# Kernel tuning notes

Measured on AMD Instinct MI355X. Metric: run time of the kernel, lower is better.

## Reference

```python
import jax, jax.numpy as jnp
import numpy as np
jax.config.update("jax_enable_x64", True)

B, S, E, H, L = 2, 1024, 768, 8, 8
FF, V = 2048, 32000
NT, REAL = 1, 512  # n_thoughts_taken, real_token_count


def _ln(x, g, b, eps=1e-5):
    m = jnp.mean(x, axis=-1, keepdims=True)
    v = jnp.var(x, axis=-1, keepdims=True)
    return (x - m) / jnp.sqrt(v + eps) * g + b


def setup_inputs() -> dict:
    key = jax.random.key(0)
    ks = jax.random.split(key, 12)
    f32 = jnp.float32
    rn = lambda k, shp, s=0.02: jax.random.normal(k, shp, f32) * s
    return {
        "x": jax.random.normal(ks[0], (B, S, E), f32),
        "tpe": rn(ks[1], (NT + 1, E)),
        "Wqkv": rn(ks[2], (L, 3 * E, E)),
        "bqkv": jnp.zeros((L, 3 * E), f32),
        "W1": rn(ks[3], (L, FF, E)),
        "b1": jnp.zeros((L, FF), f32),
        "W2": rn(ks[4], (L, E, FF)),
        "b2": jnp.zeros((L, E), f32),
        "g1": jnp.ones((L, E), f32),
        "be1": jnp.zeros((L, E), f32),
        "g2": jnp.ones((L, E), f32),
        "be2": jnp.zeros((L, E), f32),
        "gf": jnp.ones((E,), f32),
        "bf": jnp.zeros((E,), f32),
        "Wp1": rn(ks[5], (FF, E)),
        "bp1": jnp.zeros((FF,), f32),
        "Wp2": rn(ks[6], (V, FF)),
        "bp2": jnp.zeros((V,), f32),
        "Wv1": rn(ks[7], (FF, E)),
        "bv1": jnp.zeros((FF,), f32),
        "Wv2": rn(ks[8], (1, FF)),
        "bv2": jnp.zeros((1,), f32),
        "n_thoughts_taken": NT,
        "real_token_count": REAL,
    }


def reference(x, tpe, Wqkv, bqkv, W1, b1, W2, b2, g1, be1, g2, be2, gf, bf,
              Wp1, bp1, Wp2, bp2, Wv1, bv1, Wv2, bv2,
              n_thoughts_taken, real_token_count):
    Bs, Sq, Em = x.shape
    bs = int(n_thoughts_taken) + 1          # per-thought block size
    real = int(real_token_count)
    dh = Em // H

    # ---- DualPositionalEncoding (dropout=0) ----
    pos = np.arange(real)[:, None]
    div = np.exp(np.arange(0, Em, 2) * (-np.log(10000.0) / Em))
    pe = np.zeros((real, Em), np.float32)
    pe[:, 0::2] = np.sin(pos * div)
    pe[:, 1::2] = np.cos(pos * div)
    xb = x[:, :real * bs].reshape(Bs, real, bs, Em)
    xb = xb + jnp.asarray(pe)[None, :, None, :] + tpe[None, None, :bs, :]
    h = xb.reshape(Bs, real * bs, Em)
    pad = Sq - real * bs
    if pad > 0:
        h = jnp.pad(h, ((0, 0), (0, pad), (0, 0)))

    # ---- block-causal mask. NOTE: the original adds the BOOL mask to the
    # fp64 scores, so masked positions get +1.0 (not -inf). Faithful. ----
    i = np.arange(Sq)
    tok = i // bs
    p = i % bs
    M = ((tok[:, None] == tok[None, :]) & (p[None, :] >= p[:, None])) | \
        ((p[:, None] == 0) & (i[None, :] > i[:, None]) & (i[None, :] < real * bs))
    bias = jnp.asarray((M.T == 0).astype(np.float64))  # [S, S]
    scale = 1.0 / np.sqrt(dh)

    def layer(hc, params):
        Wq, bq, w1, b1_, w2, b2_, g1_, be1_, g2_, be2_ = params
        h64 = hc.astype(jnp.float64)
        qkv = h64 @ Wq.astype(jnp.float64).T + bq.astype(jnp.float64)
        q, k, v = jnp.split(qkv, 3, axis=-1)
        heads = lambda t: t.reshape(Bs, Sq, H, dh).transpose(0, 2, 1, 3)
        q, k, v = heads(q), heads(k), heads(v)
        scores = jnp.einsum('bhqd,bhkd->bhqk', q, k) * scale + bias
        w = jax.nn.softmax(scores, axis=-1)
        o = jnp.einsum('bhqk,bhkd->bhqd', w, v)
        o = o.transpose(0, 2, 1, 3).reshape(Bs, Sq, Em).astype(hc.dtype)
        # NOTE: original skips the attention out_proj entirely. Faithful.
        hc = _ln(hc + o, g1_, be1_)
        ff = jax.nn.gelu(hc @ w1.T + b1_, approximate=False) @ w2.T + b2_
        hc = _ln(hc + ff, g2_, be2_)
        return jnp.nan_to_num(hc), None

    h, _ = jax.lax.scan(layer, h, (Wqkv, bqkv, W1, b1, W2, b2, g1, be1, g2, be2))
    h = _ln(h, gf, bf)  # TransformerEncoder final norm

    act_idx = jnp.arange(real) * bs + n_thoughts_taken
    a = h[:, act_idx]  # [B, real, E]
    policy = jax.nn.gelu(a @ Wp1.T + bp1, approximate=False) @ Wp2.T + bp2
    value = jax.nn.gelu(a @ Wv1.T + bv1, approximate=False) @ Wv2.T + bv2
    return policy, value
```

## Files before the change

### kernel.cpp

```cpp
#include <hip/hip_runtime.h>
#include <math.h>

#define BB    2
#define SS    1024
#define EE    768
#define NH    8
#define DHD   96
#define NL    8
#define FFD   2048
#define VD    32000
#define REALC 512
#define MTOK  (BB*SS)
#define MACTN (BB*REALC)
#define QKVW  (3*EE)

#define QB 64
#define KB 64
#define KS_LD 104
#define VT_LD 72
#define P_LD  72

typedef __attribute__((ext_vector_type(8))) short bf16x8;
typedef __attribute__((ext_vector_type(4))) float f32x4;

static __device__ __forceinline__ float gelu_exact(float x) {
    return 0.5f * x * (1.0f + erff(x * 0.7071067811865476f));
}
static __device__ __forceinline__ unsigned short f2bf(float f) {
    unsigned int u = __builtin_bit_cast(unsigned int, f);
    unsigned int r = u + 0x7FFFu + ((u >> 16) & 1u);
    return (unsigned short)(r >> 16);
}
static __device__ __forceinline__ float bf2f(unsigned short u) {
    union { unsigned int i; float f; } v; v.i = ((unsigned int)u) << 16; return v.f;
}

#define GLDS16(gp, lp) __builtin_amdgcn_global_load_lds( \
    (const __attribute__((address_space(1))) void*)(gp), \
    (__attribute__((address_space(3))) void*)(lp), 16, 0, 0)

__global__ __launch_bounds__(256) void f2b_kernel(const float* __restrict__ src,
                                                  unsigned short* __restrict__ dst, int n4) {
    int i = blockIdx.x * 256 + threadIdx.x;
    if (i >= n4) return;
    float4 v = ((const float4*)src)[i];
    ushort4 o;
    o.x = f2bf(v.x); o.y = f2bf(v.y); o.z = f2bf(v.z); o.w = f2bf(v.w);
    ((ushort4*)dst)[i] = o;
}

__global__ __launch_bounds__(256) void embed_kernel(const float* __restrict__ x,
                                                    const float* __restrict__ tpe,
                                                    float* __restrict__ h,
                                                    unsigned short* __restrict__ hb) {
    int idx = blockIdx.x * 256 + threadIdx.x;
    if (idx >= MTOK * EE) return;
    int e = idx % EE;
    int tok = idx / EE;
    int s = tok & (SS - 1);
    int r = s >> 1;
    int p = s & 1;
    int k2 = (e >> 1) * 2;
    double div = exp((double)k2 * (-9.210340371976184 / (double)EE));
    double ang = (double)r * div;
    float pe = (e & 1) ? (float)cos(ang) : (float)sin(ang);
    float v = x[idx] + pe + tpe[p * EE + e];
    h[idx] = v;
    hb[idx] = f2bf(v);
}

template<int MODE>
__global__ __launch_bounds__(256) void gemm_bf16_kernel(
    const unsigned short* __restrict__ A, const unsigned short* __restrict__ W,
    const float* __restrict__ bias, float* __restrict__ Cf,
    unsigned short* __restrict__ Cb, unsigned short* __restrict__ CvT,
    int M, int N, int K, int ldc) {
    __shared__ unsigned short As[128 * 64];
    __shared__ unsigned short Ws[128 * 64];
    const int bm = blockIdx.y * 128;
    const int bn = blockIdx.x * 128;
    const int t = threadIdx.x;
    const int wave = t >> 6;
    const int lane = t & 63;
    const int wm = (wave >> 1) * 64;
    const int wn = (wave & 1) * 64;
    f32x4 acc[4][4] = {};

    const int srow = wave * 32 + (lane >> 3);
    const int scol = (lane & 7) * 8;
    const unsigned short* gA = A + (size_t)(bm + srow) * K + scol;
    const unsigned short* gW = W + (size_t)(bn + srow) * K + scol;

    for (int k0 = 0; k0 < K; k0 += 64) {
        __syncthreads();
#pragma unroll
        for (int i = 0; i < 4; ++i) {
            GLDS16(gA + (size_t)(i * 8) * K + k0, &As[(wave * 32 + i * 8) * 64]);
            GLDS16(gW + (size_t)(i * 8) * K + k0, &Ws[(wave * 32 + i * 8) * 64]);
        }
        __syncthreads();
#pragma unroll
        for (int ks = 0; ks < 2; ++ks) {
            bf16x8 a[4], b[4];
#pragma unroll
            for (int mi = 0; mi < 4; ++mi)
                a[mi] = *(const bf16x8*)&As[(wm + mi * 16 + (lane & 15)) * 64 + ks * 32 + (lane >> 4) * 8];
#pragma unroll
            for (int ni = 0; ni < 4; ++ni)
                b[ni] = *(const bf16x8*)&Ws[(wn + ni * 16 + (lane & 15)) * 64 + ks * 32 + (lane >> 4) * 8];
#pragma unroll
            for (int mi = 0; mi < 4; ++mi)
#pragma unroll
                for (int ni = 0; ni < 4; ++ni)
                    acc[mi][ni] = __builtin_amdgcn_mfma_f32_16x16x32_bf16(
                        a[mi], b[ni], acc[mi][ni], 0, 0, 0);
        }
    }

    const bool vpart = (MODE == 1) && (bn >= 2 * EE);
#pragma unroll
    for (int mi = 0; mi < 4; ++mi) {
#pragma unroll
        for (int ni = 0; ni < 4; ++ni) {
            const int c = bn + wn + ni * 16 + (lane & 15);
            const float bv = bias[c];
            const int rwb = bm + wm + mi * 16 + (lane >> 4) * 4;
            if (vpart) {
                ushort4 pk;
                pk.x = f2bf(acc[mi][ni][0] + bv);
                pk.y = f2bf(acc[mi][ni][1] + bv);
                pk.z = f2bf(acc[mi][ni][2] + bv);
                pk.w = f2bf(acc[mi][ni][3] + bv);
                *(ushort4*)&CvT[(size_t)(c - 2 * EE) * MTOK + rwb] = pk;
            } else {
#pragma unroll
                for (int r = 0; r < 4; ++r) {
                    float v = acc[mi][ni][r] + bv;
                    if (MODE == 3) {
                        v = gelu_exact(v);
                        Cb[(size_t)(rwb + r) * ldc + c] = f2bf(v);
                    } else if (MODE == 1) {
                        Cb[(size_t)(rwb + r) * ldc + c] = f2bf(v);
                    } else {
                        Cf[(size_t)(rwb + r) * ldc + c] = v;
                    }
                }
            }
        }
    }
}

__global__ __launch_bounds__(256, 2) void gemm_policy_kernel(
    const unsigned short* __restrict__ A, const unsigned short* __restrict__ W,
    const float* __restrict__ bias, float* __restrict__ C) {
    const int id = blockIdx.x;
    const int xcd = id & 7;
    const int rest = id >> 3;
    const int mt = rest & 7;
    const int nt = (rest >> 3) * 8 + xcd;
    if (nt >= VD / 256) return;
    const int bm = mt * 128;
    const int bn = nt * 256;
    const int K = FFD;

    __shared__ unsigned short As[128 * 64];
    __shared__ unsigned short Bs[256 * 64];
    const int t = threadIdx.x;
    const int w = t >> 6;
    const int lane = t & 63;
    const int wm = (w >> 1) * 64;
    const int wn = (w & 1) * 128;
    f32x4 acc[4][8] = {};

    const int rr8 = (w << 3) + (lane >> 3);
    const int cc8 = (lane & 7) * 8;
    const unsigned short* gA = A + (size_t)(bm + rr8) * K + cc8;
    const unsigned short* gB = W + (size_t)(bn + rr8) * K + cc8;

    for (int k0 = 0; k0 < K; k0 += 64) {
        __syncthreads();
#pragma unroll
        for (int i = 0; i < 4; ++i)
            GLDS16(gA + (size_t)(i * 32) * K + k0, &As[((w << 3) + i * 32) * 64]);
#pragma unroll
        for (int i = 0; i < 8; ++i)
            GLDS16(gB + (size_t)(i * 32) * K + k0, &Bs[((w << 3) + i * 32) * 64]);
        __syncthreads();
#pragma unroll
        for (int ks = 0; ks < 2; ++ks) {
            bf16x8 a[4], b[8];
#pragma unroll
            for (int mi = 0; mi < 4; ++mi)
                a[mi] = *(const bf16x8*)&As[(wm + mi * 16 + (lane & 15)) * 64 + ks * 32 + (lane >> 4) * 8];
#pragma unroll
            for (int ni = 0; ni < 8; ++ni)
                b[ni] = *(const bf16x8*)&Bs[(wn + ni * 16 + (lane & 15)) * 64 + ks * 32 + (lane >> 4) * 8];
#pragma unroll
            for (int mi = 0; mi < 4; ++mi)
#pragma unroll
                for (int ni = 0; ni < 8; ++ni)
                    acc[mi][ni] = __builtin_amdgcn_mfma_f32_16x16x32_bf16(
                        a[mi], b[ni], acc[mi][ni], 0, 0, 0);
        }
    }
#pragma unroll
    for (int mi = 0; mi < 4; ++mi) {
#pragma unroll
        for (int ni = 0; ni < 8; ++ni) {
            const int c = bn + wn + ni * 16 + (lane & 15);
            const float bv = bias[c];
            const int rwb = bm + wm + mi * 16 + (lane >> 4) * 4;
#pragma unroll
            for (int r = 0; r < 4; ++r)
                C[(size_t)(rwb + r) * VD + c] = acc[mi][ni][r] + bv;
        }
    }
}

__global__ __launch_bounds__(256) void attn_mfma_kernel(
    const unsigned short* __restrict__ qkvb,
    const unsigned short* __restrict__ vT,
    float* __restrict__ o) {
    __shared__ unsigned short Ks[KB * KS_LD];
    __shared__ unsigned short VTs[DHD * VT_LD];
    __shared__ unsigned short Ps[QB * P_LD];

    const int bq = blockIdx.x * QB;
    const int hh = blockIdx.y & 7;
    const int b  = blockIdx.y >> 3;
    const int t = threadIdx.x;
    const int w = t >> 6;
    const int lane = t & 63;
    const int lr = lane >> 4;
    const int lc = lane & 15;
    const float scale = 0.10206207261596577f;

    bf16x8 qa[3];
    {
        const unsigned short* qrow = qkvb + (size_t)(b * SS + bq + w * 16 + lc) * QKVW + hh * DHD;
#pragma unroll
        for (int ks = 0; ks < 3; ++ks)
            qa[ks] = *(const bf16x8*)(qrow + ks * 32 + lr * 8);
    }

    f32x4 acc_o[6] = {};
    float m_st[4], l_st[4];
#pragma unroll
    for (int r = 0; r < 4; ++r) { m_st[r] = -1e30f; l_st[r] = 0.f; }
    const int q_row = lr << 2;

    for (int kt = 0; kt < SS / KB; ++kt) {
        __syncthreads();
#pragma unroll
        for (int it = 0; it < 3; ++it) {
            int flat = it * 256 + t;
            int kr = flat / 12;
            int d8 = (flat % 12) * 8;
            *(bf16x8*)&Ks[kr * KS_LD + d8] =
                *(const bf16x8*)&qkvb[(size_t)(b * SS + kt * KB + kr) * QKVW + EE + hh * DHD + d8];
            int d  = flat >> 3;
            int k8 = (flat & 7) * 8;
            *(bf16x8*)&VTs[d * VT_LD + k8] =
                *(const bf16x8*)&vT[(size_t)(hh * DHD + d) * MTOK + b * SS + kt * KB + k8];
        }
        __syncthreads();

        f32x4 sfr[4] = {};
#pragma unroll
        for (int nf = 0; nf < 4; ++nf) {
#pragma unroll
            for (int ks = 0; ks < 3; ++ks) {
                bf16x8 kb = *(const bf16x8*)&Ks[(nf * 16 + lc) * KS_LD + ks * 32 + lr * 8];
                sfr[nf] = __builtin_amdgcn_mfma_f32_16x16x32_bf16(qa[ks], kb, sfr[nf], 0, 0, 0);
            }
        }
        const int kbase = kt * KB;
#pragma unroll
        for (int nf = 0; nf < 4; ++nf) {
            const int k = kbase + nf * 16 + lc;
#pragma unroll
            for (int r = 0; r < 4; ++r) {
                const int q = bq + w * 16 + q_row + r;
                bool allowed = (((k >> 1) == (q >> 1)) && ((q & 1) >= (k & 1))) ||
                               (((k & 1) == 0) && (q > k));
                sfr[nf][r] = sfr[nf][r] * scale + (allowed ? 0.f : 1.f);
            }
        }
        float corr[4];
#pragma unroll
        for (int r = 0; r < 4; ++r) {
            float v = fmaxf(fmaxf(sfr[0][r], sfr[1][r]), fmaxf(sfr[2][r], sfr[3][r]));
            v = fmaxf(v, __shfl_xor(v, 1)); v = fmaxf(v, __shfl_xor(v, 2));
            v = fmaxf(v, __shfl_xor(v, 4)); v = fmaxf(v, __shfl_xor(v, 8));
            float mn = fmaxf(m_st[r], v);
            corr[r] = __expf(m_st[r] - mn);
            m_st[r] = mn;
        }
        float rsum[4] = {0.f, 0.f, 0.f, 0.f};
#pragma unroll
        for (int nf = 0; nf < 4; ++nf) {
#pragma unroll
            for (int r = 0; r < 4; ++r) {
                float p = __expf(sfr[nf][r] - m_st[r]);
                rsum[r] += p;
                Ps[(w * 16 + q_row + r) * P_LD + nf * 16 + lc] = f2bf(p);
            }
        }
#pragma unroll
        for (int r = 0; r < 4; ++r) {
            float v = rsum[r];
            v += __shfl_xor(v, 1); v += __shfl_xor(v, 2);
            v += __shfl_xor(v, 4); v += __shfl_xor(v, 8);
            l_st[r] = l_st[r] * corr[r] + v;
        }
#pragma unroll
        for (int nf = 0; nf < 6; ++nf)
#pragma unroll
            for (int r = 0; r < 4; ++r)
                acc_o[nf][r] *= corr[r];
#pragma unroll
        for (int ks2 = 0; ks2 < 2; ++ks2) {
            bf16x8 pa = *(const bf16x8*)&Ps[(w * 16 + lc) * P_LD + ks2 * 32 + lr * 8];
#pragma unroll
            for (int nf = 0; nf < 6; ++nf) {
                bf16x8 vb = *(const bf16x8*)&VTs[(nf * 16 + lc) * VT_LD + ks2 * 32 + lr * 8];
                acc_o[nf] = __builtin_amdgcn_mfma_f32_16x16x32_bf16(pa, vb, acc_o[nf], 0, 0, 0);
            }
        }
    }
#pragma unroll
    for (int nf = 0; nf < 6; ++nf) {
#pragma unroll
        for (int r = 0; r < 4; ++r) {
            const int q = bq + w * 16 + q_row + r;
            o[(size_t)(b * SS + q) * EE + hh * DHD + nf * 16 + lc] = acc_o[nf][r] / l_st[r];
        }
    }
}

template<bool GATHER>
__global__ __launch_bounds__(256) void ln_kernel(const float* __restrict__ a,
                                                 const float* __restrict__ res,
                                                 const float* __restrict__ g,
                                                 const float* __restrict__ beta,
                                                 float* __restrict__ outf,
                                                 unsigned short* __restrict__ outb) {
    __shared__ float rs[256], rs2[256];
    const int row = blockIdx.x;
    const int t = threadIdx.x;
    int src = row;
    if (GATHER) src = (row >> 9) * SS + ((row & 511) << 1) + 1;
    const float* pa = a + (size_t)src * EE;
    const float* pr = res ? res + (size_t)src * EE : nullptr;
    float x[3];
    float s = 0.f, s2 = 0.f;
#pragma unroll
    for (int i = 0; i < 3; ++i) {
        int e = t + i * 256;
        float v = pa[e] + (pr ? pr[e] : 0.f);
        x[i] = v; s += v; s2 += v * v;
    }
    rs[t] = s; rs2[t] = s2; __syncthreads();
    for (int k = 128; k > 0; k >>= 1) {
        if (t < k) { rs[t] += rs[t + k]; rs2[t] += rs2[t + k]; }
        __syncthreads();
    }
    const float mean = rs[0] * (1.0f / EE);
    const float var  = rs2[0] * (1.0f / EE) - mean * mean;
    const float rstd = 1.0f / sqrtf(var + 1e-5f);
#pragma unroll
    for (int i = 0; i < 3; ++i) {
        int e = t + i * 256;
        float v = (x[i] - mean) * rstd * g[e] + beta[e];
        if (isnan(v)) v = 0.f;
        if (outf) outf[(size_t)row * EE + e] = v;
        if (outb) outb[(size_t)row * EE + e] = f2bf(v);
    }
}

__global__ __launch_bounds__(256) void value2_kernel(const unsigned short* __restrict__ v1,
                                                     const float* __restrict__ Wv2,
                                                     const float* __restrict__ bv2,
                                                     float* __restrict__ out) {
    __shared__ float red[256];
    const int row = blockIdx.x;
    const int t = threadIdx.x;
    const unsigned short* pr = v1 + (size_t)row * FFD;
    float s = 0.f;
    for (int i = t; i < FFD; i += 256) s = fmaf(bf2f(pr[i]), Wv2[i], s);
    red[t] = s; __syncthreads();
    for (int k = 128; k > 0; k >>= 1) {
        if (t < k) red[t] += red[t + k];
        __syncthreads();
    }
    if (t == 0) out[row] = red[0] + bv2[0];
}

extern "C" void kernel_launch(void* const* d_in, const int* in_sizes, int n_in,
                              void* d_out, int out_size, void* d_ws, size_t ws_size,
                              hipStream_t stream) {
    const float* x    = (const float*)d_in[0];
    const float* tpe  = (const float*)d_in[1];
    const float* Wqkv = (const float*)d_in[2];
    const float* bqkv = (const float*)d_in[3];
    const float* W1   = (const float*)d_in[4];
    const float* b1   = (const float*)d_in[5];
    const float* W2   = (const float*)d_in[6];
    const float* b2   = (const float*)d_in[7];
    const float* g1   = (const float*)d_in[8];
    const float* be1  = (const float*)d_in[9];
    const float* g2   = (const float*)d_in[10];
    const float* be2  = (const float*)d_in[11];
    const float* gf   = (const float*)d_in[12];
    const float* bf   = (const float*)d_in[13];
    const float* Wp1  = (const float*)d_in[14];
    const float* bp1  = (const float*)d_in[15];
    const float* Wp2  = (const float*)d_in[16];
    const float* bp2  = (const float*)d_in[17];
    const float* Wv1  = (const float*)d_in[18];
    const float* bv1  = (const float*)d_in[19];
    const float* Wv2  = (const float*)d_in[20];
    const float* bv2  = (const float*)d_in[21];

    float* ws  = (float*)d_ws;
    float* h   = ws;
    float* o   = h  + (size_t)MTOK * EE;
    float* hc  = o  + (size_t)MTOK * EE;
    float* ff2 = hc + (size_t)MTOK * EE;
    unsigned short* bws = (unsigned short*)(ff2 + (size_t)MTOK * EE);
    unsigned short* h_bf    = bws;
    unsigned short* hc_bf   = h_bf    + (size_t)MTOK * EE;
    unsigned short* ff1_bf  = hc_bf   + (size_t)MTOK * EE;
    unsigned short* act_bf  = ff1_bf  + (size_t)MTOK * FFD;
    unsigned short* p1_bf   = act_bf  + (size_t)MACTN * EE;
    unsigned short* qkv_bf  = p1_bf   + (size_t)MACTN * FFD;
    unsigned short* vT      = qkv_bf  + (size_t)MTOK * QKVW;
    unsigned short* wq_all  = vT      + (size_t)EE * MTOK;
    unsigned short* w1_all  = wq_all  + (size_t)NL * QKVW * EE;
    unsigned short* w2_all  = w1_all  + (size_t)NL * FFD * EE;
    unsigned short* wp1_bf  = w2_all  + (size_t)NL * EE * FFD;
    unsigned short* wv1_bf  = wp1_bf  + (size_t)FFD * EE;
    unsigned short* wp2_bf  = wv1_bf  + (size_t)FFD * EE;

    float* pol = (float*)d_out;
    float* val = (float*)d_out + (size_t)MACTN * VD;

    const int C256 = 256;
#define NBLK(n) (((n) + 255) / 256)
#define CONV(src, dst, n) f2b_kernel<<<NBLK((n) / 4), C256, 0, stream>>>(src, dst, (int)((n) / 4))

    embed_kernel<<<NBLK(MTOK * EE), C256, 0, stream>>>(x, tpe, h, h_bf);

    CONV(Wqkv, wq_all, (size_t)NL * QKVW * EE);
    CONV(W1,   w1_all, (size_t)NL * FFD * EE);
    CONV(W2,   w2_all, (size_t)NL * EE * FFD);
    CONV(Wp1,  wp1_bf, (size_t)FFD * EE);
    CONV(Wv1,  wv1_bf, (size_t)FFD * EE);
    CONV(Wp2,  wp2_bf, (size_t)VD * FFD);

    for (int l = 0; l < NL; ++l) {
        gemm_bf16_kernel<1><<<dim3(QKVW / 128, MTOK / 128), C256, 0, stream>>>(
            h_bf, wq_all + (size_t)l * QKVW * EE, bqkv + (size_t)l * QKVW,
            nullptr, qkv_bf, vT, MTOK, QKVW, EE, QKVW);
        attn_mfma_kernel<<<dim3(SS / QB, BB * NH), C256, 0, stream>>>(qkv_bf, vT, o);
        ln_kernel<false><<<MTOK, C256, 0, stream>>>(h, o, g1 + l * EE, be1 + l * EE, hc, hc_bf);
        gemm_bf16_kernel<3><<<dim3(FFD / 128, MTOK / 128), C256, 0, stream>>>(
            hc_bf, w1_all + (size_t)l * FFD * EE, b1 + (size_t)l * FFD,
            nullptr, ff1_bf, nullptr, MTOK, FFD, EE, FFD);
        gemm_bf16_kernel<0><<<dim3(EE / 128, MTOK / 128), C256, 0, stream>>>(
            ff1_bf, w2_all + (size_t)l * EE * FFD, b2 + (size_t)l * EE,
            ff2, nullptr, nullptr, MTOK, EE, FFD, EE);
        ln_kernel<false><<<MTOK, C256, 0, stream>>>(hc, ff2, g2 + l * EE, be2 + l * EE, h, h_bf);
    }

    ln_kernel<true><<<MACTN, C256, 0, stream>>>(h, nullptr, gf, bf, nullptr, act_bf);

    gemm_bf16_kernel<3><<<dim3(FFD / 128, MACTN / 128), C256, 0, stream>>>(
        act_bf, wp1_bf, bp1, nullptr, p1_bf, nullptr, MACTN, FFD, EE, FFD);
    gemm_policy_kernel<<<1024, C256, 0, stream>>>(p1_bf, wp2_bf, bp2, pol);

    gemm_bf16_kernel<3><<<dim3(FFD / 128, MACTN / 128), C256, 0, stream>>>(
        act_bf, wv1_bf, bv1, nullptr, p1_bf, nullptr, MACTN, FFD, EE, FFD);
    value2_kernel<<<MACTN, C256, 0, stream>>>(p1_bf, Wv2, bv2, val);
#undef CONV
#undef NBLK
}
```

Measured before the change: 1.589 ms.

## Merge weight conversions into one kernel and fuse policy/value head GEMMs

Six separate fp32-to-bf16 weight conversion launches are replaced by a single kernel that picks its source by index range. The policy and value first-layer GEMMs become one GEMM of width 2*FFD. This relies on Wp1 and Wv1 sitting next to each other in the bf16 buffer, with the two biases copied into a concatenated bias array. The policy GEMM occupancy hint is raised from 2 to 3, which may force register spilling. The goal is fewer launches and better GPU fill on the small head GEMMs, at the cost of strided A reads in the downstream kernels.

```diff
diff --git a/kernel.cpp b/kernel.cpp
--- a/kernel.cpp
+++ b/kernel.cpp
@@ -39,11 +39,34 @@
     (const __attribute__((address_space(1))) void*)(gp), \
     (__attribute__((address_space(3))) void*)(lp), 16, 0, 0)
 
-__global__ __launch_bounds__(256) void f2b_kernel(const float* __restrict__ src,
-                                                  unsigned short* __restrict__ dst, int n4) {
+#define CN0 (NL*QKVW*EE)
+#define CN1 (NL*FFD*EE)
+#define CN2 (NL*EE*FFD)
+#define CN3 (FFD*EE)
+#define CN4 (FFD*EE)
+#define CN5 (VD*FFD)
+#define CB0 (CN0/4)
+#define CB1 (CB0 + CN1/4)
+#define CB2 (CB1 + CN2/4)
+#define CB3 (CB2 + CN3/4)
+#define CB4 (CB3 + CN4/4)
+#define CB5 (CB4 + CN5/4)
+
+__global__ __launch_bounds__(256) void convall_kernel(
+    const float* __restrict__ s0, const float* __restrict__ s1,
+    const float* __restrict__ s2, const float* __restrict__ s3,
+    const float* __restrict__ s4, const float* __restrict__ s5,
+    unsigned short* __restrict__ dst) {
     int i = blockIdx.x * 256 + threadIdx.x;
-    if (i >= n4) return;
-    float4 v = ((const float4*)src)[i];
+    const float* src;
+    int loc;
+    if      (i < CB0) { src = s0; loc = i; }
+    else if (i < CB1) { src = s1; loc = i - CB0; }
+    else if (i < CB2) { src = s2; loc = i - CB1; }
+    else if (i < CB3) { src = s3; loc = i - CB2; }
+    else if (i < CB4) { src = s4; loc = i - CB3; }
+    else              { src = s5; loc = i - CB4; }
+    float4 v = ((const float4*)src)[loc];
     ushort4 o;
     o.x = f2bf(v.x); o.y = f2bf(v.y); o.z = f2bf(v.z); o.w = f2bf(v.w);
     ((ushort4*)dst)[i] = o;
@@ -150,9 +173,9 @@
     }
 }
 
-__global__ __launch_bounds__(256, 2) void gemm_policy_kernel(
+__global__ __launch_bounds__(256, 3) void gemm_policy_kernel(
     const unsigned short* __restrict__ A, const unsigned short* __restrict__ W,
-    const float* __restrict__ bias, float* __restrict__ C) {
+    const float* __restrict__ bias, float* __restrict__ C, int lda) {
     const int id = blockIdx.x;
     const int xcd = id & 7;
     const int rest = id >> 3;
@@ -174,14 +197,14 @@
 
     const int rr8 = (w << 3) + (lane >> 3);
     const int cc8 = (lane & 7) * 8;
-    const unsigned short* gA = A + (size_t)(bm + rr8) * K + cc8;
+    const unsigned short* gA = A + (size_t)(bm + rr8) * lda + cc8;
     const unsigned short* gB = W + (size_t)(bn + rr8) * K + cc8;
 
     for (int k0 = 0; k0 < K; k0 += 64) {
         __syncthreads();
 #pragma unroll
         for (int i = 0; i < 4; ++i)
-            GLDS16(gA + (size_t)(i * 32) * K + k0, &As[((w << 3) + i * 32) * 64]);
+            GLDS16(gA + (size_t)(i * 32) * lda + k0, &As[((w << 3) + i * 32) * 64]);
 #pragma unroll
         for (int i = 0; i < 8; ++i)
             GLDS16(gB + (size_t)(i * 32) * K + k0, &Bs[((w << 3) + i * 32) * 64]);
@@ -381,11 +404,11 @@
 __global__ __launch_bounds__(256) void value2_kernel(const unsigned short* __restrict__ v1,
                                                      const float* __restrict__ Wv2,
                                                      const float* __restrict__ bv2,
-                                                     float* __restrict__ out) {
+                                                     float* __restrict__ out, int ld) {
     __shared__ float red[256];
     const int row = blockIdx.x;
     const int t = threadIdx.x;
-    const unsigned short* pr = v1 + (size_t)row * FFD;
+    const unsigned short* pr = v1 + (size_t)row * ld;
     float s = 0.f;
     for (int i = t; i < FFD; i += 256) s = fmaf(bf2f(pr[i]), Wv2[i], s);
     red[t] = s; __syncthreads();
@@ -427,36 +450,35 @@
     float* o   = h  + (size_t)MTOK * EE;
     float* hc  = o  + (size_t)MTOK * EE;
     float* ff2 = hc + (size_t)MTOK * EE;
-    unsigned short* bws = (unsigned short*)(ff2 + (size_t)MTOK * EE);
+    float* bias_cat = ff2 + (size_t)MTOK * EE;
+    unsigned short* bws = (unsigned short*)(bias_cat + 4096);
     unsigned short* h_bf    = bws;
     unsigned short* hc_bf   = h_bf    + (size_t)MTOK * EE;
     unsigned short* ff1_bf  = hc_bf   + (size_t)MTOK * EE;
     unsigned short* act_bf  = ff1_bf  + (size_t)MTOK * FFD;
-    unsigned short* p1_bf   = act_bf  + (size_t)MACTN * EE;
-    unsigned short* qkv_bf  = p1_bf   + (size_t)MACTN * FFD;
+    unsigned short* p1v1_bf = act_bf  + (size_t)MACTN * EE;
+    unsigned short* qkv_bf  = p1v1_bf + (size_t)MACTN * 2 * FFD;
     unsigned short* vT      = qkv_bf  + (size_t)MTOK * QKVW;
     unsigned short* wq_all  = vT      + (size_t)EE * MTOK;
-    unsigned short* w1_all  = wq_all  + (size_t)NL * QKVW * EE;
-    unsigned short* w2_all  = w1_all  + (size_t)NL * FFD * EE;
-    unsigned short* wp1_bf  = w2_all  + (size_t)NL * EE * FFD;
-    unsigned short* wv1_bf  = wp1_bf  + (size_t)FFD * EE;
-    unsigned short* wp2_bf  = wv1_bf  + (size_t)FFD * EE;
+    unsigned short* w1_all  = wq_all  + (size_t)CN0;
+    unsigned short* w2_all  = w1_all  + (size_t)CN1;
+    unsigned short* wp1_bf  = w2_all  + (size_t)CN2;
+    unsigned short* wv1_bf  = wp1_bf  + (size_t)CN3;
+    unsigned short* wp2_bf  = wv1_bf  + (size_t)CN4;
+    (void)wv1_bf;
 
     float* pol = (float*)d_out;
     float* val = (float*)d_out + (size_t)MACTN * VD;
 
     const int C256 = 256;
 #define NBLK(n) (((n) + 255) / 256)
-#define CONV(src, dst, n) f2b_kernel<<<NBLK((n) / 4), C256, 0, stream>>>(src, dst, (int)((n) / 4))
 
     embed_kernel<<<NBLK(MTOK * EE), C256, 0, stream>>>(x, tpe, h, h_bf);
 
-    CONV(Wqkv, wq_all, (size_t)NL * QKVW * EE);
-    CONV(W1,   w1_all, (size_t)NL * FFD * EE);
-    CONV(W2,   w2_all, (size_t)NL * EE * FFD);
-    CONV(Wp1,  wp1_bf, (size_t)FFD * EE);
-    CONV(Wv1,  wv1_bf, (size_t)FFD * EE);
-    CONV(Wp2,  wp2_bf, (size_t)VD * FFD);
+    convall_kernel<<<CB5 / 256, C256, 0, stream>>>(Wqkv, W1, W2, Wp1, Wv1, Wp2, wq_all);
+
+    hipMemcpyAsync(bias_cat,        bp1, FFD * sizeof(float), hipMemcpyDeviceToDevice, stream);
+    hipMemcpyAsync(bias_cat + FFD,  bv1, FFD * sizeof(float), hipMemcpyDeviceToDevice, stream);
 
     for (int l = 0; l < NL; ++l) {
         gemm_bf16_kernel<1><<<dim3(QKVW / 128, MTOK / 128), C256, 0, stream>>>(
@@ -475,13 +497,11 @@
 
     ln_kernel<true><<<MACTN, C256, 0, stream>>>(h, nullptr, gf, bf, nullptr, act_bf);
 
-    gemm_bf16_kernel<3><<<dim3(FFD / 128, MACTN / 128), C256, 0, stream>>>(
-        act_bf, wp1_bf, bp1, nullptr, p1_bf, nullptr, MACTN, FFD, EE, FFD);
-    gemm_policy_kernel<<<1024, C256, 0, stream>>>(p1_bf, wp2_bf, bp2, pol);
-
-    gemm_bf16_kernel<3><<<dim3(FFD / 128, MACTN / 128), C256, 0, stream>>>(
-        act_bf, wv1_bf, bv1, nullptr, p1_bf, nullptr, MACTN, FFD, EE, FFD);
-    value2_kernel<<<MACTN, C256, 0, stream>>>(p1_bf, Wv2, bv2, val);
-#undef CONV
+    gemm_bf16_kernel<3><<<dim3(2 * FFD / 128, MACTN / 128), C256, 0, stream>>>(
+        act_bf, wp1_bf, bias_cat, nullptr, p1v1_bf, nullptr, MACTN, 2 * FFD, EE, 2 * FFD);
+
+    gemm_policy_kernel<<<1024, C256, 0, stream>>>(p1v1_bf, wp2_bf, bp2, pol, 2 * FFD);
+
+    value2_kernel<<<MACTN, C256, 0, stream>>>(p1v1_bf + FFD, Wv2, bv2, val, 2 * FFD);
 #undef NBLK
 }
```

New measurement: 1.703 ms. 7.2% more time.
